# Kernel tuning notes

Hardware: AMD Instinct MI355X
Metric: run time of the kernel (lower is better)

Reference implementation:

```python
import jax, jax.numpy as jnp
import numpy as np

B, M, S, E, LC, V, HOPS = 16, 2048, 6, 128, 512, 32000, 3
PAD = 1


def setup_inputs() -> dict:
    key = jax.random.key(0)
    ks = jax.random.split(key, 16)
    story = jax.random.randint(ks[0], (B, M, S), 0, V)
    kb_len = jax.random.randint(ks[1], (B,), 0, M - LC)
    conv_len = jax.random.randint(ks[2], (B,), 0, LC)
    hidden = jax.random.normal(ks[3], (1, B, 2 * E), jnp.float32)
    dh_outputs = jax.random.normal(ks[4], (B, LC, E), jnp.float32)
    tf_hidden = jax.random.normal(ks[5], (B, E), jnp.float32)
    query_vector = jax.random.normal(ks[6], (B, E), jnp.float32)
    global_pointer = jax.random.uniform(ks[7], (B, M), jnp.float32)
    C = jax.random.normal(ks[8], (HOPS + 1, V, E), jnp.float32) * 0.1
    C = C.at[:, PAD, :].set(0.0)  # padding_idx row is zero
    s = 0.05
    wA1 = jax.random.normal(ks[9], (2 * E, E), jnp.float32) * s
    bA1 = jnp.zeros((E,), jnp.float32)
    wA2 = jax.random.normal(ks[10], (E, E), jnp.float32) * s
    bA2 = jnp.zeros((E,), jnp.float32)
    wC1 = jax.random.normal(ks[11], (2 * E, E), jnp.float32) * s
    bC1 = jnp.zeros((E,), jnp.float32)
    wC2 = jax.random.normal(ks[12], (E, E), jnp.float32) * s
    bC2 = jnp.zeros((E,), jnp.float32)
    wf = jax.random.normal(ks[13], (2 * E, E), jnp.float32) * s
    bf = jnp.zeros((E,), jnp.float32)
    return dict(story=story, kb_len=kb_len, conv_len=conv_len, hidden=hidden,
                dh_outputs=dh_outputs, tf_hidden=tf_hidden, query_vector=query_vector,
                global_pointer=global_pointer, C=C, wA1=wA1, bA1=bA1, wA2=wA2, bA2=bA2,
                wC1=wC1, bC1=bC1, wC2=wC2, bC2=bC2, wf=wf, bf=bf)


def _lrelu(x):
    return jnp.where(x > 0, x, 0.1 * x)  # LeakyReLU(0.1)


def _mlp(x, w1, b1, w2, b2):
    return _lrelu(x @ w1 + b1) @ w2 + b2


def _add_lm(mem, kb_len, conv_len, dh):
    # mem: [B,M,E]; add dh[bi,:conv_len[bi]] into rows [kb_len, kb_len+conv_len)
    pos = jnp.arange(mem.shape[1])[None, :]            # [1,M]
    idx = pos - kb_len[:, None]                        # [B,M]
    mask = (idx >= 0) & (idx < conv_len[:, None])
    gathered = jnp.take_along_axis(dh, jnp.clip(idx, 0, dh.shape[1] - 1)[..., None], axis=1)
    return mem + jnp.where(mask[..., None], gathered, 0.0)


def reference(story, kb_len, conv_len, hidden, dh_outputs, tf_hidden,
              query_vector, global_pointer, C, wA1, bA1, wA2, bA2,
              wC1, bC1, wC2, bC2, wf, bf):
    # --- load_ent_memory: build m_story_ent (dropout off / eval mode) ---
    u = _lrelu(hidden[0] @ wf + bf)                    # hidden.squeeze(0) -> [B,E]
    tf = jnp.broadcast_to(tf_hidden[:, None, :], (B, M, E))
    m_story = []
    eC = None
    for hop in range(HOPS):
        eA = _add_lm(C[hop][story].sum(2), kb_len, conv_len, dh_outputs)       # [B,M,E]
        eA = _mlp(jnp.concatenate([eA, tf], -1), wA1, bA1, wA2, bA2)
        logit = jnp.einsum('bme,be->bm', eA, u)
        p = jax.nn.softmax(logit, axis=1)
        eC = _add_lm(C[hop + 1][story].sum(2), kb_len, conv_len, dh_outputs)   # [B,M,E]
        eC = _mlp(jnp.concatenate([eC, tf], -1), wC1, bC1, wC2, bC2)
        u = u + jnp.einsum('bme,bm->be', eC, p)
        m_story.append(eA)
    m_story.append(eC)
    # --- forward(query_vector, global_pointer) ---
    uq = query_vector
    gp = global_pointer[..., None]                     # [B,M,1]
    prob_logits = None
    prob_soft = None
    for hop in range(HOPS):
        mA = m_story[hop] * gp
        prob_logits = jnp.einsum('bme,be->bm', mA, uq)
        prob_soft = jax.nn.softmax(prob_logits, axis=1)
        mC = m_story[hop + 1] * gp
        uq = uq + jnp.einsum('bme,bm->be', mC, prob_soft)
    return (prob_soft, prob_logits)
```

## Files before the change

kernel.cpp:

```cpp
#include <hip/hip_runtime.h>
#include <math.h>

#define BB 16
#define MM 2048
#define SS 6
#define EE 128
#define LCC 512
#define VV 32000

typedef __attribute__((ext_vector_type(8))) __bf16 bf16x8;
typedef __attribute__((ext_vector_type(4))) float f32x4;

#define XS_STRIDE 264
#define HS_STRIDE 136

static __device__ inline void cvt8(const float* __restrict__ src, __bf16* __restrict__ dst) {
    const float4 a = *(const float4*)src;
    const float4 b = *(const float4*)(src + 4);
    bf16x8 o;
    o[0] = (__bf16)a.x; o[1] = (__bf16)a.y; o[2] = (__bf16)a.z; o[3] = (__bf16)a.w;
    o[4] = (__bf16)b.x; o[5] = (__bf16)b.y; o[6] = (__bf16)b.z; o[7] = (__bf16)b.w;
    *(bf16x8*)dst = o;
}

#define N_C8  (3 * VV * EE / 8)
#define N_D8  (BB * LCC * EE / 8)
#define N_T8  (BB * EE / 8)
#define N_W1  (256 * 128)
#define N_W2  (128 * 128)
#define N_PREP (N_C8 + N_D8 + N_T8 + N_W1 + N_W2)

__global__ __launch_bounds__(256)
void megaprep(const float* __restrict__ C, const float* __restrict__ dh,
              const float* __restrict__ tf, const float* __restrict__ W1,
              const float* __restrict__ W2,
              __bf16* __restrict__ Cb, __bf16* __restrict__ dhb,
              __bf16* __restrict__ tfb, __bf16* __restrict__ w1t,
              __bf16* __restrict__ w2t)
{
    int i = blockIdx.x * 256 + threadIdx.x;
    if (i < N_C8) { cvt8(C + (size_t)i * 8, Cb + (size_t)i * 8); return; }
    i -= N_C8;
    if (i < N_D8) { cvt8(dh + (size_t)i * 8, dhb + (size_t)i * 8); return; }
    i -= N_D8;
    if (i < N_T8) { cvt8(tf + i * 8, tfb + i * 8); return; }
    i -= N_T8;
    if (i < N_W1) { const int n = i >> 8, k = i & 255; w1t[i] = (__bf16)W1[k * EE + n]; return; }
    i -= N_W1;
    if (i < N_W2) { const int n = i >> 7, k = i & 127; w2t[i] = (__bf16)W2[k * EE + n]; }
}

__global__ __launch_bounds__(256, 8)
void embed_mlp_mfma(const int* __restrict__ story,
                    const int* __restrict__ kb_len,
                    const int* __restrict__ conv_len,
                    const __bf16* __restrict__ Cb,
                    const __bf16* __restrict__ dhb,
                    const __bf16* __restrict__ tfb,
                    const __bf16* __restrict__ w1t, const float* __restrict__ b1,
                    const __bf16* __restrict__ w2t, const float* __restrict__ b2,
                    const float* __restrict__ gp, const float* __restrict__ query,
                    __bf16* __restrict__ mout, float* __restrict__ lbuf0)
{
    __shared__ __bf16 Xs[32 * XS_STRIDE];
    __shared__ int    sidx[32 * SS];
    __bf16* Hs   = Xs;
    float*  plog = (float*)Xs;

    const int bid  = blockIdx.x;
    const int hop  = bid >> 10;
    const int row0 = (bid & 1023) * 32;
    const int b    = row0 >> 11;
    const int tid  = threadIdx.x;

    const __bf16* Ck = Cb + (size_t)hop * VV * EE;

    for (int i = tid; i < 32 * SS; i += 256) sidx[i] = story[(size_t)row0 * SS + i];

    const int kb   = kb_len[b];
    const int cl   = conv_len[b];
    const int rgrp = tid >> 4;
    const int e8   = (tid & 15) * 8;
    const bf16x8 tf8 = *(const bf16x8*)&tfb[b * EE + e8];
    __syncthreads();

    bf16x8 g[2][SS], dv[2];
    #pragma unroll
    for (int p = 0; p < 2; ++p) {
        const int r = p * 16 + rgrp;
        const int* si = &sidx[r * SS];
        #pragma unroll
        for (int s = 0; s < SS; ++s)
            g[p][s] = *(const bf16x8*)&Ck[(size_t)si[s] * EE + e8];
        const int j = ((row0 + r) & (MM - 1)) - kb;
        if (j >= 0 && j < cl) {
            dv[p] = *(const bf16x8*)&dhb[((size_t)b * LCC + j) * EE + e8];
        } else {
            bf16x8 z;
            #pragma unroll
            for (int q = 0; q < 8; ++q) z[q] = (__bf16)0.f;
            dv[p] = z;
        }
    }
    #pragma unroll
    for (int p = 0; p < 2; ++p) {
        const int r = p * 16 + rgrp;
        bf16x8 pk;
        #pragma unroll
        for (int q = 0; q < 8; ++q) {
            float s = (float)dv[p][q];
            #pragma unroll
            for (int s6 = 0; s6 < SS; ++s6) s += (float)g[p][s6][q];
            pk[q] = (__bf16)s;
        }
        *(bf16x8*)&Xs[r * XS_STRIDE + e8]      = pk;
        *(bf16x8*)&Xs[r * XS_STRIDE + EE + e8] = tf8;
    }
    __syncthreads();

    const int w       = tid >> 6;
    const int lane    = tid & 63;
    const int lr      = lane & 15;
    const int lk      = lane >> 4;
    const int colbase = w * 32;

    f32x4 acc1[2][2];
    #pragma unroll
    for (int i = 0; i < 2; ++i)
        #pragma unroll
        for (int j = 0; j < 2; ++j) acc1[i][j] = (f32x4){0.f, 0.f, 0.f, 0.f};

    for (int ks = 0; ks < 8; ++ks) {
        bf16x8 a[2], bw[2];
        #pragma unroll
        for (int mt = 0; mt < 2; ++mt)
            a[mt] = *(const bf16x8*)&Xs[(mt * 16 + lr) * XS_STRIDE + ks * 32 + lk * 8];
        #pragma unroll
        for (int nt = 0; nt < 2; ++nt)
            bw[nt] = *(const bf16x8*)&w1t[(size_t)(colbase + nt * 16 + lr) * 256 + ks * 32 + lk * 8];
        #pragma unroll
        for (int mt = 0; mt < 2; ++mt)
            #pragma unroll
            for (int nt = 0; nt < 2; ++nt)
                acc1[mt][nt] = __builtin_amdgcn_mfma_f32_16x16x32_bf16(a[mt], bw[nt], acc1[mt][nt], 0, 0, 0);
    }
    __syncthreads();
    {
        const float b1v[2] = { b1[colbase + lr], b1[colbase + 16 + lr] };
        #pragma unroll
        for (int mt = 0; mt < 2; ++mt)
            #pragma unroll
            for (int nt = 0; nt < 2; ++nt)
                #pragma unroll
                for (int reg = 0; reg < 4; ++reg) {
                    float h = acc1[mt][nt][reg] + b1v[nt];
                    h = (h > 0.f) ? h : 0.1f * h;
                    Hs[(mt * 16 + lk * 4 + reg) * HS_STRIDE + colbase + nt * 16 + lr] = (__bf16)h;
                }
    }
    __syncthreads();

    f32x4 acc2[2][2];
    #pragma unroll
    for (int i = 0; i < 2; ++i)
        #pragma unroll
        for (int j = 0; j < 2; ++j) acc2[i][j] = (f32x4){0.f, 0.f, 0.f, 0.f};

    for (int ks = 0; ks < 4; ++ks) {
        bf16x8 a[2], bw[2];
        #pragma unroll
        for (int mt = 0; mt < 2; ++mt)
            a[mt] = *(const bf16x8*)&Hs[(mt * 16 + lr) * HS_STRIDE + ks * 32 + lk * 8];
        #pragma unroll
        for (int nt = 0; nt < 2; ++nt)
            bw[nt] = *(const bf16x8*)&w2t[(size_t)(colbase + nt * 16 + lr) * 128 + ks * 32 + lk * 8];
        #pragma unroll
        for (int mt = 0; mt < 2; ++mt)
            #pragma unroll
            for (int nt = 0; nt < 2; ++nt)
                acc2[mt][nt] = __builtin_amdgcn_mfma_f32_16x16x32_bf16(a[mt], bw[nt], acc2[mt][nt], 0, 0, 0);
    }

    const float b2v[2] = { b2[colbase + lr], b2[colbase + 16 + lr] };

    if (hop == 0) {
        const float qv0 = query[b * EE + colbase + lr];
        const float qv1 = query[b * EE + colbase + 16 + lr];
        __syncthreads();
        #pragma unroll
        for (int mt = 0; mt < 2; ++mt)
            #pragma unroll
            for (int reg = 0; reg < 4; ++reg) {
                float p = (acc2[mt][0][reg] + b2v[0]) * qv0
                        + (acc2[mt][1][reg] + b2v[1]) * qv1;
                p += __shfl_xor(p, 1, 64);
                p += __shfl_xor(p, 2, 64);
                p += __shfl_xor(p, 4, 64);
                p += __shfl_xor(p, 8, 64);
                if (lr == 0) plog[(mt * 16 + lk * 4 + reg) * 4 + w] = p;
            }
        __syncthreads();
        if (tid < 32) {
            const float l = plog[tid * 4] + plog[tid * 4 + 1] + plog[tid * 4 + 2] + plog[tid * 4 + 3];
            lbuf0[row0 + tid] = l * gp[row0 + tid];
        }
    } else {
        __bf16* out = mout + (size_t)(hop - 1) * 32768 * EE;
        #pragma unroll
        for (int mt = 0; mt < 2; ++mt)
            #pragma unroll
            for (int nt = 0; nt < 2; ++nt)
                #pragma unroll
                for (int reg = 0; reg < 4; ++reg) {
                    const int rg_ = row0 + mt * 16 + lk * 4 + reg;
                    out[(size_t)rg_ * EE + colbase + nt * 16 + lr] =
                        (__bf16)(acc2[mt][nt][reg] + b2v[nt]);
                }
    }
}

__global__ __launch_bounds__(1024)
void tail_kernel(const __bf16* __restrict__ m, const float* __restrict__ gp,
                 const float* __restrict__ lbuf0, const float* __restrict__ query,
                 float* __restrict__ out_logits, float* __restrict__ out_soft)
{
    __shared__ float uqs[128];
    __shared__ float wls[2048];
    __shared__ float lls[2048];
    __shared__ float part[16][128];
    __shared__ float redm[16], reds[16];

    const int b    = blockIdx.x;
    const int tid  = threadIdx.x;
    const int w    = tid >> 6;
    const int lane = tid & 63;
    const int g    = lane >> 4;
    const int l16  = lane & 15;
    const float* gpb = gp + (size_t)b * MM;

    if (tid < 128) uqs[tid] = query[b * EE + tid];
    lls[tid]        = lbuf0[(size_t)b * MM + tid];
    lls[tid + 1024] = lbuf0[(size_t)b * MM + tid + 1024];
    __syncthreads();

    for (int hop = 0; hop < 3; ++hop) {
        const float v0 = lls[tid], v1 = lls[tid + 1024];
        float mx = fmaxf(v0, v1);
        #pragma unroll
        for (int off = 32; off > 0; off >>= 1) mx = fmaxf(mx, __shfl_xor(mx, off, 64));
        if (lane == 0) redm[w] = mx;
        __syncthreads();
        float bmx = redm[0];
        #pragma unroll
        for (int i = 1; i < 16; ++i) bmx = fmaxf(bmx, redm[i]);
        const float e0 = __expf(v0 - bmx), e1 = __expf(v1 - bmx);
        float sm = e0 + e1;
        #pragma unroll
        for (int off = 32; off > 0; off >>= 1) sm += __shfl_xor(sm, off, 64);
        if (lane == 0) reds[w] = sm;
        __syncthreads();
        float bs = 0.f;
        #pragma unroll
        for (int i = 0; i < 16; ++i) bs += reds[i];
        const float inv = 1.f / bs;

        if (hop == 2) {
            out_soft[(size_t)b * MM + tid]        = e0 * inv;
            out_soft[(size_t)b * MM + tid + 1024] = e1 * inv;
            return;
        }
        wls[tid]        = e0 * inv * gpb[tid];
        wls[tid + 1024] = e1 * inv * gpb[tid + 1024];
        __syncthreads();

        const __bf16* mh = m + ((size_t)hop * 32768 + (size_t)b * MM) * EE;

        float acc[8];
        #pragma unroll
        for (int q = 0; q < 8; ++q) acc[q] = 0.f;
        for (int it = 0; it < 32; ++it) {
            const int row = w * 128 + it * 4 + g;
            const bf16x8 mv = *(const bf16x8*)&mh[(size_t)row * EE + l16 * 8];
            const float wg = wls[row];
            #pragma unroll
            for (int q = 0; q < 8; ++q) acc[q] += wg * (float)mv[q];
        }
        #pragma unroll
        for (int q = 0; q < 8; ++q) {
            acc[q] += __shfl_xor(acc[q], 16, 64);
            acc[q] += __shfl_xor(acc[q], 32, 64);
        }
        if (lane < 16) {
            #pragma unroll
            for (int q = 0; q < 8; ++q) part[w][l16 * 8 + q] = acc[q];
        }
        __syncthreads();
        if (tid < 128) {
            float s = uqs[tid];
            #pragma unroll
            for (int ww = 0; ww < 16; ++ww) s += part[ww][tid];
            uqs[tid] = s;
        }
        __syncthreads();

        float u[8];
        #pragma unroll
        for (int j = 0; j < 8; ++j) u[j] = uqs[l16 * 8 + j];
        for (int it = 0; it < 32; ++it) {
            const int row = w * 128 + it * 4 + g;
            const bf16x8 mv = *(const bf16x8*)&mh[(size_t)row * EE + l16 * 8];
            float p = 0.f;
            #pragma unroll
            for (int j = 0; j < 8; ++j) p += (float)mv[j] * u[j];
            p += __shfl_xor(p, 1, 64);
            p += __shfl_xor(p, 2, 64);
            p += __shfl_xor(p, 4, 64);
            p += __shfl_xor(p, 8, 64);
            if (l16 == 0) {
                const float lv = p * gpb[row];
                lls[row] = lv;
                if (hop == 1) out_logits[(size_t)b * MM + row] = lv;
            }
        }
        __syncthreads();
    }
}

extern "C" void kernel_launch(void* const* d_in, const int* in_sizes, int n_in,
                              void* d_out, int out_size, void* d_ws, size_t ws_size,
                              hipStream_t stream) {
    const int*   story    = (const int*)d_in[0];
    const int*   kb_len   = (const int*)d_in[1];
    const int*   conv_len = (const int*)d_in[2];
    const float* dh       = (const float*)d_in[4];
    const float* tf       = (const float*)d_in[5];
    const float* query    = (const float*)d_in[6];
    const float* gp       = (const float*)d_in[7];
    const float* C        = (const float*)d_in[8];
    const float* wA1      = (const float*)d_in[9];
    const float* bA1      = (const float*)d_in[10];
    const float* wA2      = (const float*)d_in[11];
    const float* bA2      = (const float*)d_in[12];

    char* ws = (char*)d_ws;
    const size_t M_ELEMS = (size_t)32768 * EE;
    size_t off = 0;
    __bf16* m   = (__bf16*)(ws + off); off += 2 * M_ELEMS * sizeof(__bf16);
    __bf16* Cb  = (__bf16*)(ws + off); off += (size_t)3 * VV * EE * sizeof(__bf16);
    __bf16* dhb = (__bf16*)(ws + off); off += (size_t)BB * LCC * EE * sizeof(__bf16);
    __bf16* tfb = (__bf16*)(ws + off); off += (size_t)BB * EE * sizeof(__bf16);
    __bf16* w1t = (__bf16*)(ws + off); off += 256 * 128 * sizeof(__bf16);
    __bf16* w2t = (__bf16*)(ws + off); off += 128 * 128 * sizeof(__bf16);
    float* lbuf = (float*)(ws + off);  off += (size_t)BB * MM * sizeof(float);

    float* out_soft   = (float*)d_out;
    float* out_logits = out_soft + (size_t)BB * MM;

    megaprep<<<N_PREP / 256, 256, 0, stream>>>(C, dh, tf, wA1, wA2,
                                               Cb, dhb, tfb, w1t, w2t);
    embed_mlp_mfma<<<3072, 256, 0, stream>>>(story, kb_len, conv_len, Cb, dhb, tfb,
                                             w1t, bA1, w2t, bA2, gp, query, m, lbuf);
    tail_kernel<<<BB, 1024, 0, stream>>>(m, gp, lbuf, query, out_logits, out_soft);
}
```

Before: 239.2 us.

## Split tail across 256 blocks with grid barriers and stage memory rows in LDS

Replaces the 16-block tail kernel (one block per batch) with a 256-block kernel that gives each block a 128-row segment. Hop updates to the query vector are accumulated with global atomics, and phases are separated by a software grid barrier whose counters are reset in the prep kernel. The embed kernel also gets a separate Hs buffer instead of aliasing Xs, which removes one __syncthreads but raises LDS use and drops the occupancy hint. The grid barrier relies on all 256 blocks being co-resident without a cooperative launch, and atomic float accumulation changes summation order.

```diff
diff --git a/kernel.cpp b/kernel.cpp
--- a/kernel.cpp
+++ b/kernel.cpp
@@ -7,12 +7,14 @@
 #define EE 128
 #define LCC 512
 #define VV 32000
+#define NTB 256
 
 typedef __attribute__((ext_vector_type(8))) __bf16 bf16x8;
 typedef __attribute__((ext_vector_type(4))) float f32x4;
 
 #define XS_STRIDE 264
 #define HS_STRIDE 136
+#define MS_STRIDE 136
 
 static __device__ inline void cvt8(const float* __restrict__ src, __bf16* __restrict__ dst) {
     const float4 a = *(const float4*)src;
@@ -28,15 +30,17 @@
 #define N_T8  (BB * EE / 8)
 #define N_W1  (256 * 128)
 #define N_W2  (128 * 128)
-#define N_PREP (N_C8 + N_D8 + N_T8 + N_W1 + N_W2)
+#define N_UQ  (BB * EE)
+#define N_PREP (N_C8 + N_D8 + N_T8 + N_W1 + N_W2 + N_UQ + 256)
 
 __global__ __launch_bounds__(256)
 void megaprep(const float* __restrict__ C, const float* __restrict__ dh,
               const float* __restrict__ tf, const float* __restrict__ W1,
-              const float* __restrict__ W2,
+              const float* __restrict__ W2, const float* __restrict__ query,
               __bf16* __restrict__ Cb, __bf16* __restrict__ dhb,
               __bf16* __restrict__ tfb, __bf16* __restrict__ w1t,
-              __bf16* __restrict__ w2t)
+              __bf16* __restrict__ w2t, float* __restrict__ uqA,
+              float* __restrict__ uqB, unsigned* __restrict__ syncv)
 {
     int i = blockIdx.x * 256 + threadIdx.x;
     if (i < N_C8) { cvt8(C + (size_t)i * 8, Cb + (size_t)i * 8); return; }
@@ -47,10 +51,14 @@
     i -= N_T8;
     if (i < N_W1) { const int n = i >> 8, k = i & 255; w1t[i] = (__bf16)W1[k * EE + n]; return; }
     i -= N_W1;
-    if (i < N_W2) { const int n = i >> 7, k = i & 127; w2t[i] = (__bf16)W2[k * EE + n]; }
-}
-
-__global__ __launch_bounds__(256, 8)
+    if (i < N_W2) { const int n = i >> 7, k = i & 127; w2t[i] = (__bf16)W2[k * EE + n]; return; }
+    i -= N_W2;
+    if (i < N_UQ) { uqA[i] = query[i]; uqB[i] = 0.f; return; }
+    i -= N_UQ;
+    if (i < 2) syncv[i] = 0u;
+}
+
+__global__ __launch_bounds__(256)
 void embed_mlp_mfma(const int* __restrict__ story,
                     const int* __restrict__ kb_len,
                     const int* __restrict__ conv_len,
@@ -63,9 +71,9 @@
                     __bf16* __restrict__ mout, float* __restrict__ lbuf0)
 {
     __shared__ __bf16 Xs[32 * XS_STRIDE];
+    __shared__ __bf16 Hs[32 * HS_STRIDE];
     __shared__ int    sidx[32 * SS];
-    __bf16* Hs   = Xs;
-    float*  plog = (float*)Xs;
+    float* plog = (float*)Hs;
 
     const int bid  = blockIdx.x;
     const int hop  = bid >> 10;
@@ -144,7 +152,6 @@
             for (int nt = 0; nt < 2; ++nt)
                 acc1[mt][nt] = __builtin_amdgcn_mfma_f32_16x16x32_bf16(a[mt], bw[nt], acc1[mt][nt], 0, 0, 0);
     }
-    __syncthreads();
     {
         const float b1v[2] = { b1[colbase + lr], b1[colbase + 16 + lr] };
         #pragma unroll
@@ -219,18 +226,45 @@
     }
 }
 
-__global__ __launch_bounds__(1024)
-void tail_kernel(const __bf16* __restrict__ m, const float* __restrict__ gp,
-                 const float* __restrict__ lbuf0, const float* __restrict__ query,
-                 float* __restrict__ out_logits, float* __restrict__ out_soft)
+static __device__ inline void gridbar(unsigned* cnt, unsigned* gen,
+                                      unsigned target, int tid)
 {
+    __syncthreads();
+    if (tid == 0) {
+        __threadfence();
+        const unsigned arr =
+            __hip_atomic_fetch_add(cnt, 1u, __ATOMIC_ACQ_REL, __HIP_MEMORY_SCOPE_AGENT) + 1;
+        if (arr == NTB) {
+            __hip_atomic_store(cnt, 0u, __ATOMIC_RELAXED, __HIP_MEMORY_SCOPE_AGENT);
+            __hip_atomic_fetch_add(gen, 1u, __ATOMIC_ACQ_REL, __HIP_MEMORY_SCOPE_AGENT);
+        } else {
+            while (__hip_atomic_load(gen, __ATOMIC_ACQUIRE, __HIP_MEMORY_SCOPE_AGENT) < target) {
+                __builtin_amdgcn_s_sleep(1);
+            }
+        }
+    }
+    __syncthreads();
+}
+
+__global__ __launch_bounds__(256)
+void tail_coop(const __bf16* __restrict__ m, const float* __restrict__ gp,
+               const float* __restrict__ lbuf0, float* __restrict__ lbuf1,
+               float* __restrict__ uqA, float* __restrict__ uqB,
+               unsigned* __restrict__ syncv,
+               float* __restrict__ out_logits, float* __restrict__ out_soft)
+{
+    __shared__ __bf16 Ms[128 * MS_STRIDE];
     __shared__ float uqs[128];
-    __shared__ float wls[2048];
-    __shared__ float lls[2048];
-    __shared__ float part[16][128];
-    __shared__ float redm[16], reds[16];
-
-    const int b    = blockIdx.x;
+    __shared__ float wls[128];
+    __shared__ float redm[4], reds[4];
+    __shared__ float part[4][128];
+
+    unsigned* cnt = syncv;
+    unsigned* gen = syncv + 1;
+
+    const int b    = blockIdx.x >> 4;
+    const int seg  = blockIdx.x & 15;
+    const int rlo  = seg * 128;
     const int tid  = threadIdx.x;
     const int w    = tid >> 6;
     const int lane = tid & 63;
@@ -238,92 +272,129 @@
     const int l16  = lane & 15;
     const float* gpb = gp + (size_t)b * MM;
 
-    if (tid < 128) uqs[tid] = query[b * EE + tid];
-    lls[tid]        = lbuf0[(size_t)b * MM + tid];
-    lls[tid + 1024] = lbuf0[(size_t)b * MM + tid + 1024];
-    __syncthreads();
-
-    for (int hop = 0; hop < 3; ++hop) {
-        const float v0 = lls[tid], v1 = lls[tid + 1024];
-        float mx = fmaxf(v0, v1);
-        #pragma unroll
-        for (int off = 32; off > 0; off >>= 1) mx = fmaxf(mx, __shfl_xor(mx, off, 64));
-        if (lane == 0) redm[w] = mx;
-        __syncthreads();
-        float bmx = redm[0];
-        #pragma unroll
-        for (int i = 1; i < 16; ++i) bmx = fmaxf(bmx, redm[i]);
-        const float e0 = __expf(v0 - bmx), e1 = __expf(v1 - bmx);
-        float sm = e0 + e1;
-        #pragma unroll
-        for (int off = 32; off > 0; off >>= 1) sm += __shfl_xor(sm, off, 64);
-        if (lane == 0) reds[w] = sm;
-        __syncthreads();
-        float bs = 0.f;
-        #pragma unroll
-        for (int i = 0; i < 16; ++i) bs += reds[i];
-        const float inv = 1.f / bs;
-
-        if (hop == 2) {
-            out_soft[(size_t)b * MM + tid]        = e0 * inv;
-            out_soft[(size_t)b * MM + tid + 1024] = e1 * inv;
-            return;
-        }
-        wls[tid]        = e0 * inv * gpb[tid];
-        wls[tid + 1024] = e1 * inv * gpb[tid + 1024];
-        __syncthreads();
-
-        const __bf16* mh = m + ((size_t)hop * 32768 + (size_t)b * MM) * EE;
-
-        float acc[8];
-        #pragma unroll
-        for (int q = 0; q < 8; ++q) acc[q] = 0.f;
-        for (int it = 0; it < 32; ++it) {
-            const int row = w * 128 + it * 4 + g;
-            const bf16x8 mv = *(const bf16x8*)&mh[(size_t)row * EE + l16 * 8];
-            const float wg = wls[row];
-            #pragma unroll
-            for (int q = 0; q < 8; ++q) acc[q] += wg * (float)mv[q];
-        }
-        #pragma unroll
-        for (int q = 0; q < 8; ++q) {
-            acc[q] += __shfl_xor(acc[q], 16, 64);
-            acc[q] += __shfl_xor(acc[q], 32, 64);
-        }
-        if (lane < 16) {
-            #pragma unroll
-            for (int q = 0; q < 8; ++q) part[w][l16 * 8 + q] = acc[q];
-        }
-        __syncthreads();
-        if (tid < 128) {
-            float s = uqs[tid];
-            #pragma unroll
-            for (int ww = 0; ww < 16; ++ww) s += part[ww][tid];
-            uqs[tid] = s;
-        }
-        __syncthreads();
-
-        float u[8];
-        #pragma unroll
-        for (int j = 0; j < 8; ++j) u[j] = uqs[l16 * 8 + j];
-        for (int it = 0; it < 32; ++it) {
-            const int row = w * 128 + it * 4 + g;
-            const bf16x8 mv = *(const bf16x8*)&mh[(size_t)row * EE + l16 * 8];
-            float p = 0.f;
-            #pragma unroll
-            for (int j = 0; j < 8; ++j) p += (float)mv[j] * u[j];
-            p += __shfl_xor(p, 1, 64);
-            p += __shfl_xor(p, 2, 64);
-            p += __shfl_xor(p, 4, 64);
-            p += __shfl_xor(p, 8, 64);
-            if (l16 == 0) {
-                const float lv = p * gpb[row];
-                lls[row] = lv;
-                if (hop == 1) out_logits[(size_t)b * MM + row] = lv;
-            }
-        }
-        __syncthreads();
-    }
+    float mx, inv;
+
+    #define STATS2048(LB)                                                      \
+        {                                                                      \
+            float v_[8]; float m_ = -1e30f;                                    \
+            _Pragma("unroll")                                                  \
+            for (int i_ = 0; i_ < 8; ++i_) {                                   \
+                v_[i_] = (LB)[i_ * 256 + tid]; m_ = fmaxf(m_, v_[i_]);         \
+            }                                                                  \
+            _Pragma("unroll")                                                  \
+            for (int o_ = 32; o_ > 0; o_ >>= 1)                                \
+                m_ = fmaxf(m_, __shfl_xor(m_, o_, 64));                        \
+            if (lane == 0) redm[w] = m_;                                       \
+            __syncthreads();                                                   \
+            mx = fmaxf(fmaxf(redm[0], redm[1]), fmaxf(redm[2], redm[3]));      \
+            float s_ = 0.f;                                                    \
+            _Pragma("unroll")                                                  \
+            for (int i_ = 0; i_ < 8; ++i_) s_ += __expf(v_[i_] - mx);          \
+            _Pragma("unroll")                                                  \
+            for (int o_ = 32; o_ > 0; o_ >>= 1) s_ += __shfl_xor(s_, o_, 64);  \
+            if (lane == 0) reds[w] = s_;                                       \
+            __syncthreads();                                                   \
+            inv = 1.f / (reds[0] + reds[1] + reds[2] + reds[3]);               \
+        }
+
+    #define LOAD_MS(HOPIDX)                                                    \
+        {                                                                      \
+            const __bf16* mb_ = m + ((size_t)(HOPIDX) * (BB * MM)              \
+                                     + (size_t)b * MM + rlo) * EE;             \
+            for (int i_ = tid; i_ < 128 * 16; i_ += 256) {                     \
+                const int r_ = i_ >> 4, c_ = (i_ & 15) * 8;                    \
+                *(bf16x8*)&Ms[r_ * MS_STRIDE + c_] =                           \
+                    *(const bf16x8*)&mb_[(size_t)r_ * EE + c_];                \
+            }                                                                  \
+        }
+
+    #define UPDATE_PHASE(UQ)                                                   \
+        {                                                                      \
+            float acc_[8];                                                     \
+            _Pragma("unroll")                                                  \
+            for (int q_ = 0; q_ < 8; ++q_) acc_[q_] = 0.f;                     \
+            _Pragma("unroll")                                                  \
+            for (int it_ = 0; it_ < 8; ++it_) {                                \
+                const int row_ = w * 32 + it_ * 4 + g;                         \
+                const float wg_ = wls[row_];                                   \
+                const bf16x8 mv_ = *(const bf16x8*)&Ms[row_ * MS_STRIDE + l16 * 8]; \
+                _Pragma("unroll")                                              \
+                for (int q_ = 0; q_ < 8; ++q_) acc_[q_] += wg_ * (float)mv_[q_]; \
+            }                                                                  \
+            _Pragma("unroll")                                                  \
+            for (int q_ = 0; q_ < 8; ++q_) {                                   \
+                acc_[q_] += __shfl_xor(acc_[q_], 16, 64);                      \
+                acc_[q_] += __shfl_xor(acc_[q_], 32, 64);                      \
+            }                                                                  \
+            if (lane < 16) {                                                   \
+                _Pragma("unroll")                                              \
+                for (int q_ = 0; q_ < 8; ++q_) part[w][l16 * 8 + q_] = acc_[q_]; \
+            }                                                                  \
+            __syncthreads();                                                   \
+            if (tid < 128) {                                                   \
+                const float s_ = part[0][tid] + part[1][tid]                   \
+                               + part[2][tid] + part[3][tid];                  \
+                atomicAdd(&(UQ)[b * EE + tid], s_);                            \
+            }                                                                  \
+        }
+
+    #define LOGITS_PHASE(DST)                                                  \
+        {                                                                      \
+            float u_[8];                                                       \
+            _Pragma("unroll")                                                  \
+            for (int j_ = 0; j_ < 8; ++j_) u_[j_] = uqs[l16 * 8 + j_];         \
+            _Pragma("unroll")                                                  \
+            for (int it_ = 0; it_ < 8; ++it_) {                                \
+                const int row_ = w * 32 + it_ * 4 + g;                         \
+                const bf16x8 mv_ = *(const bf16x8*)&Ms[row_ * MS_STRIDE + l16 * 8]; \
+                float p_ = 0.f;                                                \
+                _Pragma("unroll")                                              \
+                for (int j_ = 0; j_ < 8; ++j_) p_ += (float)mv_[j_] * u_[j_];  \
+                p_ += __shfl_xor(p_, 1, 64);                                   \
+                p_ += __shfl_xor(p_, 2, 64);                                   \
+                p_ += __shfl_xor(p_, 4, 64);                                   \
+                p_ += __shfl_xor(p_, 8, 64);                                   \
+                if (l16 == 0)                                                  \
+                    (DST)[(size_t)b * MM + rlo + row_] = p_ * gpb[rlo + row_]; \
+            }                                                                  \
+        }
+
+    LOAD_MS(0);
+    STATS2048(lbuf0 + (size_t)b * MM);
+    if (tid < 128)
+        wls[tid] = __expf(lbuf0[(size_t)b * MM + rlo + tid] - mx) * inv * gpb[rlo + tid];
+    __syncthreads();
+    UPDATE_PHASE(uqA);
+    gridbar(cnt, gen, 1, tid);
+
+    if (tid < 128) uqs[tid] = uqA[b * EE + tid];
+    __syncthreads();
+    LOGITS_PHASE(lbuf1);
+    gridbar(cnt, gen, 2, tid);
+
+    LOAD_MS(1);
+    STATS2048(lbuf1 + (size_t)b * MM);
+    if (tid < 128)
+        wls[tid] = __expf(lbuf1[(size_t)b * MM + rlo + tid] - mx) * inv * gpb[rlo + tid];
+    __syncthreads();
+    UPDATE_PHASE(uqB);
+    gridbar(cnt, gen, 3, tid);
+
+    if (tid < 128) uqs[tid] = uqA[b * EE + tid] + uqB[b * EE + tid];
+    __syncthreads();
+    LOGITS_PHASE(out_logits);
+    gridbar(cnt, gen, 4, tid);
+
+    STATS2048(out_logits + (size_t)b * MM);
+    if (tid < 128) {
+        const int r = rlo + tid;
+        out_soft[(size_t)b * MM + r] =
+            __expf(out_logits[(size_t)b * MM + r] - mx) * inv;
+    }
+    #undef STATS2048
+    #undef LOAD_MS
+    #undef UPDATE_PHASE
+    #undef LOGITS_PHASE
 }
 
 extern "C" void kernel_launch(void* const* d_in, const int* in_sizes, int n_in,
@@ -351,14 +422,20 @@
     __bf16* tfb = (__bf16*)(ws + off); off += (size_t)BB * EE * sizeof(__bf16);
     __bf16* w1t = (__bf16*)(ws + off); off += 256 * 128 * sizeof(__bf16);
     __bf16* w2t = (__bf16*)(ws + off); off += 128 * 128 * sizeof(__bf16);
-    float* lbuf = (float*)(ws + off);  off += (size_t)BB * MM * sizeof(float);
+    float* lbuf0 = (float*)(ws + off); off += (size_t)BB * MM * sizeof(float);
+    float* lbuf1 = (float*)(ws + off); off += (size_t)BB * MM * sizeof(float);
+    float* uqA   = (float*)(ws + off); off += (size_t)BB * EE * sizeof(float);
+    float* uqB   = (float*)(ws + off); off += (size_t)BB * EE * sizeof(float);
+    unsigned* syncv = (unsigned*)(ws + off); off += 64;
 
     float* out_soft   = (float*)d_out;
     float* out_logits = out_soft + (size_t)BB * MM;
 
-    megaprep<<<N_PREP / 256, 256, 0, stream>>>(C, dh, tf, wA1, wA2,
-                                               Cb, dhb, tfb, w1t, w2t);
+    megaprep<<<(N_PREP + 255) / 256, 256, 0, stream>>>(C, dh, tf, wA1, wA2, query,
+                                                       Cb, dhb, tfb, w1t, w2t,
+                                                       uqA, uqB, syncv);
     embed_mlp_mfma<<<3072, 256, 0, stream>>>(story, kb_len, conv_len, Cb, dhb, tfb,
-                                             w1t, bA1, w2t, bA2, gp, query, m, lbuf);
-    tail_kernel<<<BB, 1024, 0, stream>>>(m, gp, lbuf, query, out_logits, out_soft);
-}
+                                             w1t, bA1, w2t, bA2, gp, query, m, lbuf0);
+    tail_coop<<<NTB, 256, 0, stream>>>(m, gp, lbuf0, lbuf1, uqA, uqB, syncv,
+                                       out_logits, out_soft);
+}
```

Result: slower. 287.8 us (+20.3%).
